# Optimization experiments

Hardware: AMD Instinct MI355X
Metric: run time of the kernel (lower is better)

Reference implementation:

```python
import jax, jax.numpy as jnp
import numpy as np

N = 50000            # nodes (cells)
E_RAND = 1_600_000   # random edges; self loops appended -> E = E_RAND + N
DIMS = [(512, 384), (384, 256), (256, 128)]  # (in, hidden) per encoder stage
OUT = 128


def setup_inputs() -> dict:
    key = jax.random.key(0)
    ks = jax.random.split(key, 16)
    features = jax.random.normal(ks[0], (N, DIMS[0][0]), dtype=jnp.float32)
    src = jax.random.randint(ks[1], (E_RAND,), 0, N, dtype=jnp.int32)
    dst = jax.random.randint(ks[2], (E_RAND,), 0, N, dtype=jnp.int32)
    loops = jnp.arange(N, dtype=jnp.int32)  # dgl.add_self_loop
    src = jnp.concatenate([src, loops])
    dst = jnp.concatenate([dst, loops])
    inp = {"features": features, "src": src, "dst": dst}
    i = 3
    for s, (din, dout) in enumerate(DIMS):
        inp[f"sage_w{s}"] = jax.random.normal(ks[i], (dout, din), jnp.float32) / np.sqrt(din); i += 1
        inp[f"sage_b{s}"] = jnp.zeros((dout,), jnp.float32)
        inp[f"gc_w{s}"] = jax.random.normal(ks[i], (dout, dout), jnp.float32) / np.sqrt(dout); i += 1
        inp[f"gc_b{s}"] = jnp.zeros((dout,), jnp.float32)
    inp["fc_w"] = jax.random.normal(ks[i], (OUT, DIMS[-1][1]), jnp.float32) / np.sqrt(DIMS[-1][1])
    inp["fc_b"] = jnp.zeros((OUT,), jnp.float32)
    return inp


def reference(features, src, dst,
              sage_w0, sage_b0, gc_w0, gc_b0,
              sage_w1, sage_b1, gc_w1, gc_b1,
              sage_w2, sage_b2, gc_w2, gc_b2,
              fc_w, fc_b):
    ones = jnp.ones((src.shape[0],), jnp.float32)
    in_deg = jax.ops.segment_sum(ones, dst, num_segments=N)
    out_deg = jax.ops.segment_sum(ones, src, num_segments=N)
    # GraphConv norm='both' scalers (clamp degree to >=1, as DGL does)
    inv_src = jnp.where(out_deg > 0, out_deg, 1.0) ** -0.5  # [N]
    inv_dst = jnp.where(in_deg > 0, in_deg, 1.0) ** -0.5    # [N]
    sage_den = (in_deg + 1.0)[:, None]                      # SAGE 'gcn' denominator

    def sage_gcn(h, w, b):
        # DGL SAGEConv aggregator_type='gcn': (sum_neigh + self)/(in_deg+1) -> fc_neigh
        agg = jax.ops.segment_sum(h[src], dst, num_segments=N)
        return ((agg + h) / sage_den) @ w.T + b

    def graph_conv(h, w, b):
        # DGL GraphConv norm='both': D_out^{-1/2} -> sum aggregate -> D_in^{-1/2} -> W
        hn = h * inv_src[:, None]
        agg = jax.ops.segment_sum(hn[src], dst, num_segments=N)
        return (agg * inv_dst[:, None]) @ w.T + b

    params = [(sage_w0, sage_b0, gc_w0, gc_b0),
              (sage_w1, sage_b1, gc_w1, gc_b1),
              (sage_w2, sage_b2, gc_w2, gc_b2)]
    h = features
    for sw, sb, gw, gb in params:
        h = jax.nn.relu(sage_gcn(h, sw, sb))
        h = jax.nn.relu(graph_conv(h, gw, gb))
    return h @ fc_w.T + fc_b
```

## Files before the change

kernel.cpp:

```cpp
#include <hip/hip_runtime.h>
#include <cstddef>
#include <cstdint>


typedef _Float16 h8 __attribute__((ext_vector_type(8)));
typedef _Float16 h4 __attribute__((ext_vector_type(4)));
typedef float f32x4 __attribute__((ext_vector_type(4)));

#define GLD_LDS16(gptr, lptr)                                                  \
  __builtin_amdgcn_global_load_lds(                                            \
      (const __attribute__((address_space(1))) void*)(gptr),                   \
      (__attribute__((address_space(3))) void*)(lptr), 16, 0, 0)


__global__ __launch_bounds__(256) void deg_kernel(
    const int* __restrict__ src, const int* __restrict__ dst,
    int* __restrict__ in_deg, int* __restrict__ out_deg, int E) {
  int e = blockIdx.x * 256 + threadIdx.x;
  if (e < E) {
    atomicAdd(&in_deg[dst[e]], 1);
    atomicAdd(&out_deg[src[e]], 1);
  }
}

__global__ __launch_bounds__(1024) void scan_kernel(
    const int* __restrict__ deg, int* __restrict__ row_ptr, int n) {
  __shared__ int buf[1024];
  __shared__ int carry_s;
  if (threadIdx.x == 0) carry_s = 0;
  __syncthreads();
  for (int base = 0; base < n; base += 1024) {
    int i = base + (int)threadIdx.x;
    int v = (i < n) ? ((deg[i] + 3) & ~3) : 0;
    buf[threadIdx.x] = v;
    __syncthreads();
    #pragma unroll
    for (int off = 1; off < 1024; off <<= 1) {
      int t = 0;
      if ((int)threadIdx.x >= off) t = buf[threadIdx.x - off];
      __syncthreads();
      buf[threadIdx.x] += t;
      __syncthreads();
    }
    int incl  = buf[threadIdx.x];
    int carry = carry_s;
    int total = buf[1023];
    __syncthreads();
    if (i < n) row_ptr[i] = carry + incl - v;
    if (threadIdx.x == 0) carry_s = carry + total;
    __syncthreads();
  }
  if (threadIdx.x == 0) row_ptr[n] = carry_s;
}

__global__ __launch_bounds__(256) void scatter_kernel(
    const int* __restrict__ src, const int* __restrict__ dst,
    const int* __restrict__ row_ptr, int* __restrict__ cnt,
    int* __restrict__ csr, int E) {
  int e = blockIdx.x * 256 + threadIdx.x;
  if (e < E) {
    int d = dst[e];
    int pos = row_ptr[d] + atomicAdd(&cnt[d], 1);
    csr[pos] = src[e];
  }
}

__global__ __launch_bounds__(256) void pad_fill_kernel(
    const int* __restrict__ row_ptr, const int* __restrict__ deg,
    int* __restrict__ csr, int n, int dummy) {
  int i = blockIdx.x * 256 + threadIdx.x;
  if (i < n) {
    int s = row_ptr[i] + deg[i], e = row_ptr[i + 1];
    for (int p = s; p < e; ++p) csr[p] = dummy;
  }
}

__global__ __launch_bounds__(256) void scaler_kernel(
    const int* __restrict__ in_deg, const int* __restrict__ out_deg,
    float* __restrict__ inv_src, float* __restrict__ inv_dst,
    float* __restrict__ inv_den, int n) {
  int i = blockIdx.x * 256 + threadIdx.x;
  if (i < n) {
    float od = (float)out_deg[i];
    float id = (float)in_deg[i];
    inv_src[i] = rsqrtf(od > 0.f ? od : 1.0f);
    inv_dst[i] = rsqrtf(id > 0.f ? id : 1.0f);
    inv_den[i] = 1.0f / (id + 1.0f);
  }
}


__global__ __launch_bounds__(256) void cvt_kernel(
    const float* __restrict__ in, _Float16* __restrict__ out,
    long n_in, long n_pad) {
  long i = ((long)blockIdx.x * 256 + (long)threadIdx.x) * 4;
  if (i >= n_pad) return;
  float4 v = (i < n_in) ? *(const float4*)(in + i) : make_float4(0.f, 0.f, 0.f, 0.f);
  h4 h = {(_Float16)v.x, (_Float16)v.y, (_Float16)v.z, (_Float16)v.w};
  *(h4*)(out + i) = h;
}


template <typename OutT>
__global__ __launch_bounds__(256) void hgemm(
    const _Float16* __restrict__ A, const _Float16* __restrict__ W,
    OutT* __restrict__ C, int Mstore, int K, int Nc,
    const float* __restrict__ row_scale, const float* __restrict__ bias) {
  __shared__ _Float16 As[128 * 32];
  __shared__ _Float16 Bs[128 * 32];
  const int tid = threadIdx.x;
  const int bm = blockIdx.x * 128, bn = blockIdx.y * 128;
  const int wave = tid >> 6, lane = tid & 63;
  const int wm = (wave & 1) * 64, wn = (wave >> 1) * 64;
  const int lrow = lane & 15, lq = lane >> 4;

  const int colh = (lane & 3) * 8;
  const int arow = wave * 16 + (lane >> 2);
  const _Float16* Ag  = A + (size_t)(bm + arow) * K + colh;
  const _Float16* Ag2 = A + (size_t)(bm + 64 + arow) * K + colh;
  const _Float16* Wg  = W + (size_t)(bn + arow) * K + colh;
  const _Float16* Wg2 = W + (size_t)(bn + 64 + arow) * K + colh;
  _Float16* lA  = As + wave * 512;
  _Float16* lA2 = As + 64 * 32 + wave * 512;
  _Float16* lB  = Bs + wave * 512;
  _Float16* lB2 = Bs + 64 * 32 + wave * 512;

  f32x4 acc[4][4];
  #pragma unroll
  for (int i = 0; i < 4; ++i)
    #pragma unroll
    for (int j = 0; j < 4; ++j) acc[i][j] = (f32x4){0.f, 0.f, 0.f, 0.f};

  for (int k0 = 0; k0 < K; k0 += 32) {
    __syncthreads();
    GLD_LDS16(Ag + k0, lA);
    GLD_LDS16(Ag2 + k0, lA2);
    GLD_LDS16(Wg + k0, lB);
    GLD_LDS16(Wg2 + k0, lB2);
    __syncthreads();
    h8 af[4], bf[4];
    #pragma unroll
    for (int i = 0; i < 4; ++i)
      af[i] = *(const h8*)(As + (wm + i * 16 + lrow) * 32 + lq * 8);
    #pragma unroll
    for (int j = 0; j < 4; ++j)
      bf[j] = *(const h8*)(Bs + (wn + j * 16 + lrow) * 32 + lq * 8);
    #pragma unroll
    for (int i = 0; i < 4; ++i)
      #pragma unroll
      for (int j = 0; j < 4; ++j)
        acc[i][j] = __builtin_amdgcn_mfma_f32_16x16x32_f16(af[i], bf[j], acc[i][j], 0, 0, 0);
  }

  #pragma unroll
  for (int i = 0; i < 4; ++i) {
    #pragma unroll
    for (int r = 0; r < 4; ++r) {
      const int m = bm + wm + i * 16 + lq * 4 + r;
      if (m < Mstore) {
        const float rsc = row_scale ? row_scale[m] : 1.0f;
        OutT* crow = C + (size_t)m * Nc + bn + wn + lrow;
        #pragma unroll
        for (int j = 0; j < 4; ++j) {
          float v = acc[i][j][r] * rsc;
          if (bias) v += bias[bn + wn + j * 16 + lrow];
          crow[j * 16] = (OutT)v;
        }
      }
    }
  }
}


template <int D, bool SELF>
__global__ __launch_bounds__(256) void agg_h(
    const _Float16* __restrict__ Z, const int* __restrict__ row_ptr,
    const int* __restrict__ csr, const float* __restrict__ out_scale,
    const float* __restrict__ bias, _Float16* __restrict__ out, int n) {
  constexpr int GROUP = 16;
  constexpr int NV = D / 8 / GROUP;
  const int gid = threadIdx.x >> 4;
  const int lane = threadIdx.x & 15;
  const int node = blockIdx.x * 16 + gid;
  if (node >= n) return;

  const int rs = row_ptr[node], re = row_ptr[node + 1];

  float acc[NV][8];
  #pragma unroll
  for (int v = 0; v < NV; ++v)
    #pragma unroll
    for (int q = 0; q < 8; ++q) acc[v][q] = 0.f;

  for (int e = rs; e < re; e += GROUP) {
    int m = re - e; if (m > GROUP) m = GROUP;
    int eid = (e + lane < re) ? csr[e + lane] : 0;
    for (int j = 0; j < m; j += 4) {
      const int s0 = __shfl(eid, j + 0, GROUP);
      const int s1 = __shfl(eid, j + 1, GROUP);
      const int s2 = __shfl(eid, j + 2, GROUP);
      const int s3 = __shfl(eid, j + 3, GROUP);
      const h8* z0 = (const h8*)(Z + (size_t)s0 * D);
      const h8* z1 = (const h8*)(Z + (size_t)s1 * D);
      const h8* z2 = (const h8*)(Z + (size_t)s2 * D);
      const h8* z3 = (const h8*)(Z + (size_t)s3 * D);
      h8 t0[NV], t1[NV], t2[NV], t3[NV];
      #pragma unroll
      for (int v = 0; v < NV; ++v) {
        const int idx = lane + v * GROUP;
        t0[v] = z0[idx]; t1[v] = z1[idx]; t2[v] = z2[idx]; t3[v] = z3[idx];
      }
      #pragma unroll
      for (int v = 0; v < NV; ++v)
        #pragma unroll
        for (int q = 0; q < 8; ++q)
          acc[v][q] += ((float)t0[v][q] + (float)t1[v][q]) +
                       ((float)t2[v][q] + (float)t3[v][q]);
    }
  }

  const float osc = out_scale[node];
  const h8* zs = (const h8*)(Z + (size_t)node * D);
  _Float16* orow = out + (size_t)node * D;
  #pragma unroll
  for (int v = 0; v < NV; ++v) {
    const int idx = lane + v * GROUP;
    if (SELF) {
      h8 t = zs[idx];
      #pragma unroll
      for (int q = 0; q < 8; ++q) acc[v][q] += (float)t[q];
    }
    h8 r;
    #pragma unroll
    for (int q = 0; q < 8; ++q) {
      float x = acc[v][q] * osc + bias[idx * 8 + q];
      r[q] = (_Float16)fmaxf(x, 0.f);
    }
    *(h8*)(orow + idx * 8) = r;
  }
}


static void launch_cvt(const float* in, _Float16* out, long n_in, long n_pad,
                       hipStream_t st) {
  long thr = n_pad / 4;
  cvt_kernel<<<(int)((thr + 255) / 256), 256, 0, st>>>(in, out, n_in, n_pad);
}

extern "C" void kernel_launch(void* const* d_in, const int* in_sizes, int n_in,
                              void* d_out, int out_size, void* d_ws, size_t ws_size,
                              hipStream_t stream) {
  const float* features = (const float*)d_in[0];
  const int*   src      = (const int*)d_in[1];
  const int*   dst      = (const int*)d_in[2];
  const float* wsrc[7] = {(const float*)d_in[3],  (const float*)d_in[5],
                          (const float*)d_in[7],  (const float*)d_in[9],
                          (const float*)d_in[11], (const float*)d_in[13],
                          (const float*)d_in[15]};
  const float* sb[3] = {(const float*)d_in[4],  (const float*)d_in[8],  (const float*)d_in[12]};
  const float* gb[3] = {(const float*)d_in[6],  (const float*)d_in[10], (const float*)d_in[14]};
  const float* fc_b  = (const float*)d_in[16];

  const int N = in_sizes[0] / 512;
  const int E = in_sizes[1];
  const int MB = (N + 127) / 128;
  const int Mpad = MB * 128;
  const int Epad_max = E + 3 * N + 64;

  const int wcnt[7] = {384 * 512, 384 * 384, 256 * 384, 256 * 256,
                       128 * 256, 128 * 128, 128 * 128};

  char* ws = (char*)d_ws;
  _Float16* featH = (_Float16*)ws;
  _Float16* hA    = featH + (size_t)Mpad * 512;
  _Float16* hB    = hA + (size_t)Mpad * 384;
  _Float16* wH[7];
  {
    _Float16* p = hB + (size_t)(Mpad + 1) * 384;
    for (int i = 0; i < 7; ++i) { wH[i] = p; p += wcnt[i]; }
  }
  int* csr     = (int*)(wH[6] + wcnt[6]);
  int* rp      = csr + Epad_max;
  int* in_dg   = rp + (N + 1);
  int* out_dg  = in_dg + N;
  int* cnt     = out_dg + N;
  float* inv_src = (float*)(cnt + N);
  float* inv_dst = inv_src + N;
  float* inv_den = inv_dst + N;

  size_t totw = 0; for (int i = 0; i < 7; ++i) totw += wcnt[i];
  size_t needed = ((size_t)Mpad * (512 + 384) + (size_t)(Mpad + 1) * 384 + totw) * 2 +
                  ((size_t)Epad_max + (N + 1) + 6 * (size_t)N) * 4;
  if (ws_size < needed) return;

  (void)hipMemsetAsync(in_dg, 0, sizeof(int) * 3 * (size_t)N, stream);
  (void)hipMemsetAsync(hA + (size_t)N * 384, 0, (size_t)(Mpad - N) * 384 * 2, stream);

  const int eb = (E + 255) / 256;
  const int nb = (N + 255) / 256;
  deg_kernel<<<eb, 256, 0, stream>>>(src, dst, in_dg, out_dg, E);
  scan_kernel<<<1, 1024, 0, stream>>>(in_dg, rp, N);
  scatter_kernel<<<eb, 256, 0, stream>>>(src, dst, rp, cnt, csr, E);
  pad_fill_kernel<<<nb, 256, 0, stream>>>(rp, in_dg, csr, N, Mpad);
  scaler_kernel<<<nb, 256, 0, stream>>>(in_dg, out_dg, inv_src, inv_dst, inv_den, N);

  launch_cvt(features, featH, (long)N * 512, (long)Mpad * 512, stream);
  for (int i = 0; i < 7; ++i) launch_cvt(wsrc[i], wH[i], wcnt[i], wcnt[i], stream);

  const int dout[3] = {384, 256, 128};
  const _Float16* h = featH;
  int K = 512;
  for (int s = 0; s < 3; ++s) {
    const int D = dout[s];
    dim3 gg(MB, D / 128);
    const int ab = (N + 15) / 16;
    (void)hipMemsetAsync(hB + (size_t)Mpad * D, 0, (size_t)D * 2, stream);
    hgemm<_Float16><<<gg, 256, 0, stream>>>(h, wH[2 * s], hB, Mpad, K, D, nullptr, nullptr);
    if (D == 384)      agg_h<384, true><<<ab, 256, 0, stream>>>(hB, rp, csr, inv_den, sb[s], hA, N);
    else if (D == 256) agg_h<256, true><<<ab, 256, 0, stream>>>(hB, rp, csr, inv_den, sb[s], hA, N);
    else               agg_h<128, true><<<ab, 256, 0, stream>>>(hB, rp, csr, inv_den, sb[s], hA, N);
    hgemm<_Float16><<<gg, 256, 0, stream>>>(hA, wH[2 * s + 1], hB, Mpad, D, D, inv_src, nullptr);
    if (D == 384)      agg_h<384, false><<<ab, 256, 0, stream>>>(hB, rp, csr, inv_dst, gb[s], hA, N);
    else if (D == 256) agg_h<256, false><<<ab, 256, 0, stream>>>(hB, rp, csr, inv_dst, gb[s], hA, N);
    else               agg_h<128, false><<<ab, 256, 0, stream>>>(hB, rp, csr, inv_dst, gb[s], hA, N);
    h = hA;
    K = D;
  }
  dim3 gf(MB, 1);
  hgemm<float><<<gf, 256, 0, stream>>>(h, wH[6], (float*)d_out, N, 128, 128, nullptr, fc_b);
}
```

Measured before the change: 1.368 ms.

## Slice neighbor aggregation by feature columns and store CSR indices as uint16

```diff
diff --git a/kernel.cpp b/kernel.cpp
--- a/kernel.cpp
+++ b/kernel.cpp
@@ -56,22 +56,22 @@
 __global__ __launch_bounds__(256) void scatter_kernel(
     const int* __restrict__ src, const int* __restrict__ dst,
     const int* __restrict__ row_ptr, int* __restrict__ cnt,
-    int* __restrict__ csr, int E) {
+    unsigned short* __restrict__ csr, int E) {
   int e = blockIdx.x * 256 + threadIdx.x;
   if (e < E) {
     int d = dst[e];
     int pos = row_ptr[d] + atomicAdd(&cnt[d], 1);
-    csr[pos] = src[e];
+    csr[pos] = (unsigned short)src[e];
   }
 }
 
 __global__ __launch_bounds__(256) void pad_fill_kernel(
     const int* __restrict__ row_ptr, const int* __restrict__ deg,
-    int* __restrict__ csr, int n, int dummy) {
+    unsigned short* __restrict__ csr, int n, int dummy) {
   int i = blockIdx.x * 256 + threadIdx.x;
   if (i < n) {
     int s = row_ptr[i] + deg[i], e = row_ptr[i + 1];
-    for (int p = s; p < e; ++p) csr[p] = dummy;
+    for (int p = s; p < e; ++p) csr[p] = (unsigned short)dummy;
   }
 }
 
@@ -173,70 +173,63 @@
 
 
 template <int D, bool SELF>
-__global__ __launch_bounds__(256) void agg_h(
+__global__ __launch_bounds__(256) void agg_slice(
     const _Float16* __restrict__ Z, const int* __restrict__ row_ptr,
-    const int* __restrict__ csr, const float* __restrict__ out_scale,
+    const unsigned short* __restrict__ csr, const float* __restrict__ out_scale,
     const float* __restrict__ bias, _Float16* __restrict__ out, int n) {
-  constexpr int GROUP = 16;
-  constexpr int NV = D / 8 / GROUP;
   const int gid = threadIdx.x >> 4;
-  const int lane = threadIdx.x & 15;
+  const int l = threadIdx.x & 15;
   const int node = blockIdx.x * 16 + gid;
+  const int sb = blockIdx.y * 32;
   if (node >= n) return;
 
   const int rs = row_ptr[node], re = row_ptr[node + 1];
-
-  float acc[NV][8];
+  const int c = l & 3;
+  const int j = l >> 2;
+
+  float acc[8];
   #pragma unroll
-  for (int v = 0; v < NV; ++v)
-    #pragma unroll
-    for (int q = 0; q < 8; ++q) acc[v][q] = 0.f;
-
-  for (int e = rs; e < re; e += GROUP) {
-    int m = re - e; if (m > GROUP) m = GROUP;
-    int eid = (e + lane < re) ? csr[e + lane] : 0;
-    for (int j = 0; j < m; j += 4) {
-      const int s0 = __shfl(eid, j + 0, GROUP);
-      const int s1 = __shfl(eid, j + 1, GROUP);
-      const int s2 = __shfl(eid, j + 2, GROUP);
-      const int s3 = __shfl(eid, j + 3, GROUP);
-      const h8* z0 = (const h8*)(Z + (size_t)s0 * D);
-      const h8* z1 = (const h8*)(Z + (size_t)s1 * D);
-      const h8* z2 = (const h8*)(Z + (size_t)s2 * D);
-      const h8* z3 = (const h8*)(Z + (size_t)s3 * D);
-      h8 t0[NV], t1[NV], t2[NV], t3[NV];
+  for (int q = 0; q < 8; ++q) acc[q] = 0.f;
+
+  const _Float16* Zs = Z + sb + c * 8;
+
+  for (int e = rs; e < re; e += 16) {
+    int m = re - e; if (m > 16) m = 16;
+    int eid = (e + l < re) ? (int)csr[e + l] : 0;
+    const int nq = m >> 2;
+    int sid[4];
+    #pragma unroll
+    for (int q = 0; q < 4; ++q) sid[q] = __shfl(eid, q * 4 + j, 16);
+    h8 t[4];
+    #pragma unroll
+    for (int q = 0; q < 4; ++q)
+      if (q < nq) t[q] = *(const h8*)(Zs + (size_t)sid[q] * D);
+    #pragma unroll
+    for (int q = 0; q < 4; ++q)
+      if (q < nq)
+        #pragma unroll
+        for (int k = 0; k < 8; ++k) acc[k] += (float)t[q][k];
+  }
+
+  #pragma unroll
+  for (int k = 0; k < 8; ++k) {
+    acc[k] += __shfl_xor(acc[k], 4, 16);
+    acc[k] += __shfl_xor(acc[k], 8, 16);
+  }
+
+  if (j == 0) {
+    const float osc = out_scale[node];
+    if (SELF) {
+      h8 t = *(const h8*)(Zs + (size_t)node * D);
       #pragma unroll
-      for (int v = 0; v < NV; ++v) {
-        const int idx = lane + v * GROUP;
-        t0[v] = z0[idx]; t1[v] = z1[idx]; t2[v] = z2[idx]; t3[v] = z3[idx];
-      }
-      #pragma unroll
-      for (int v = 0; v < NV; ++v)
-        #pragma unroll
-        for (int q = 0; q < 8; ++q)
-          acc[v][q] += ((float)t0[v][q] + (float)t1[v][q]) +
-                       ((float)t2[v][q] + (float)t3[v][q]);
+      for (int k = 0; k < 8; ++k) acc[k] += (float)t[k];
     }
-  }
-
-  const float osc = out_scale[node];
-  const h8* zs = (const h8*)(Z + (size_t)node * D);
-  _Float16* orow = out + (size_t)node * D;
-  #pragma unroll
-  for (int v = 0; v < NV; ++v) {
-    const int idx = lane + v * GROUP;
-    if (SELF) {
-      h8 t = zs[idx];
-      #pragma unroll
-      for (int q = 0; q < 8; ++q) acc[v][q] += (float)t[q];
-    }
+    const float* bp = bias + sb + c * 8;
     h8 r;
     #pragma unroll
-    for (int q = 0; q < 8; ++q) {
-      float x = acc[v][q] * osc + bias[idx * 8 + q];
-      r[q] = (_Float16)fmaxf(x, 0.f);
-    }
-    *(h8*)(orow + idx * 8) = r;
+    for (int k = 0; k < 8; ++k)
+      r[k] = (_Float16)fmaxf(acc[k] * osc + bp[k], 0.f);
+    *(h8*)(out + (size_t)node * D + sb + c * 8) = r;
   }
 }
 
@@ -279,18 +272,18 @@
     _Float16* p = hB + (size_t)(Mpad + 1) * 384;
     for (int i = 0; i < 7; ++i) { wH[i] = p; p += wcnt[i]; }
   }
-  int* csr     = (int*)(wH[6] + wcnt[6]);
-  int* rp      = csr + Epad_max;
+  int* rp      = (int*)(wH[6] + wcnt[6]);
   int* in_dg   = rp + (N + 1);
   int* out_dg  = in_dg + N;
   int* cnt     = out_dg + N;
   float* inv_src = (float*)(cnt + N);
   float* inv_dst = inv_src + N;
   float* inv_den = inv_dst + N;
+  unsigned short* csr = (unsigned short*)(inv_den + N);
 
   size_t totw = 0; for (int i = 0; i < 7; ++i) totw += wcnt[i];
   size_t needed = ((size_t)Mpad * (512 + 384) + (size_t)(Mpad + 1) * 384 + totw) * 2 +
-                  ((size_t)Epad_max + (N + 1) + 6 * (size_t)N) * 4;
+                  ((size_t)(N + 1) + 6 * (size_t)N) * 4 + (size_t)Epad_max * 2;
   if (ws_size < needed) return;
 
   (void)hipMemsetAsync(in_dg, 0, sizeof(int) * 3 * (size_t)N, stream);
@@ -313,16 +306,16 @@
   for (int s = 0; s < 3; ++s) {
     const int D = dout[s];
     dim3 gg(MB, D / 128);
-    const int ab = (N + 15) / 16;
+    dim3 ga((N + 15) / 16, D / 32);
     (void)hipMemsetAsync(hB + (size_t)Mpad * D, 0, (size_t)D * 2, stream);
     hgemm<_Float16><<<gg, 256, 0, stream>>>(h, wH[2 * s], hB, Mpad, K, D, nullptr, nullptr);
-    if (D == 384)      agg_h<384, true><<<ab, 256, 0, stream>>>(hB, rp, csr, inv_den, sb[s], hA, N);
-    else if (D == 256) agg_h<256, true><<<ab, 256, 0, stream>>>(hB, rp, csr, inv_den, sb[s], hA, N);
-    else               agg_h<128, true><<<ab, 256, 0, stream>>>(hB, rp, csr, inv_den, sb[s], hA, N);
+    if (D == 384)      agg_slice<384, true><<<ga, 256, 0, stream>>>(hB, rp, csr, inv_den, sb[s], hA, N);
+    else if (D == 256) agg_slice<256, true><<<ga, 256, 0, stream>>>(hB, rp, csr, inv_den, sb[s], hA, N);
+    else               agg_slice<128, true><<<ga, 256, 0, stream>>>(hB, rp, csr, inv_den, sb[s], hA, N);
     hgemm<_Float16><<<gg, 256, 0, stream>>>(hA, wH[2 * s + 1], hB, Mpad, D, D, inv_src, nullptr);
-    if (D == 384)      agg_h<384, false><<<ab, 256, 0, stream>>>(hB, rp, csr, inv_dst, gb[s], hA, N);
-    else if (D == 256) agg_h<256, false><<<ab, 256, 0, stream>>>(hB, rp, csr, inv_dst, gb[s], hA, N);
-    else               agg_h<128, false><<<ab, 256, 0, stream>>>(hB, rp, csr, inv_dst, gb[s], hA, N);
+    if (D == 384)      agg_slice<384, false><<<ga, 256, 0, stream>>>(hB, rp, csr, inv_dst, gb[s], hA, N);
+    else if (D == 256) agg_slice<256, false><<<ga, 256, 0, stream>>>(hB, rp, csr, inv_dst, gb[s], hA, N);
+    else               agg_slice<128, false><<<ga, 256, 0, stream>>>(hB, rp, csr, inv_dst, gb[s], hA, N);
     h = hA;
     K = D;
   }
```

Result: slower. 1.491 ms (+9.0%).
